# Optimization experiments

Measured on AMD Instinct MI355X. Metric: run time of the kernel, lower is better.

Reference implementation:

```python
import jax, jax.numpy as jnp
import numpy as np

NW, NT, ND, D = 30000, 2000, 20000, 128
E = {'ww': 600000, 'wt': 300000, 'wd': 400000, 'td': 100000, 'tt': 40000}
ENDS = {'ww': (NW, NW), 'wt': (NW, NT), 'wd': (NW, ND), 'td': (NT, ND), 'tt': (NT, NT)}


def setup_inputs() -> dict:
    key = jax.random.key(0)
    ks = iter(jax.random.split(key, 64))
    nrm = lambda shape: jax.random.normal(next(ks), shape, dtype=jnp.float32)
    inp = {}
    inp['feat_word'] = nrm((NW, D))
    inp['feat_topic'] = nrm((NT, D))
    # 'effect' node data: ~half the topics are causal (nonzero effect)
    inp['effect'] = jax.random.randint(next(ks), (NT,), 0, 2).astype(jnp.float32)
    # independent Bernoulli(0.1) draws for the td and tt iterations
    inp['bern_td'] = (jax.random.uniform(next(ks), (NT,)) < 0.1).astype(jnp.float32)
    inp['bern_tt'] = (jax.random.uniform(next(ks), (NT,)) < 0.1).astype(jnp.float32)
    for et, (ns, nd) in ENDS.items():
        inp[f'src_{et}'] = jax.random.randint(next(ks), (E[et],), 0, ns, dtype=jnp.int32)
        inp[f'dst_{et}'] = jax.random.randint(next(ks), (E[et],), 0, nd, dtype=jnp.int32)
        inp[f'w_{et}'] = jax.random.uniform(next(ks), (E[et],), dtype=jnp.float32)
    for name in ['ww', 'wt', 'wd', 'td', 'tt']:
        inp[f'W_{name}'] = nrm((D, D)) * 0.05
        inp[f'b_{name}'] = jnp.zeros((D,), jnp.float32)
    inp['W_causal'] = nrm((D, D)) * 0.05
    inp['W_noise'] = nrm((D, D)) * 0.05
    inp['n_doc'] = ND
    return inp


def _mean_agg(Wh, w, src, dst, n_dst):
    # DGL fn.u_mul_e + fn.mean: mean of (Wh[src]*w) over incoming edges; 0 for isolated dst
    m = Wh[src] * w[:, None]                                    # [E, D]
    s = jax.ops.segment_sum(m, dst, num_segments=n_dst)          # [n_dst, D]
    deg = jax.ops.segment_sum(jnp.ones_like(w), dst, num_segments=n_dst)
    return jnp.where(deg[:, None] > 0, s / jnp.maximum(deg, 1.0)[:, None], 0.0)


def reference(feat_word, feat_topic, effect, bern_td, bern_tt,
              src_ww, dst_ww, w_ww, src_wt, dst_wt, w_wt,
              src_wd, dst_wd, w_wd, src_td, dst_td, w_td,
              src_tt, dst_tt, w_tt,
              W_ww, b_ww, W_wt, b_wt, W_wd, b_wd, W_td, b_td, W_tt, b_tt,
              W_causal, W_noise, n_doc):
    n_word, n_topic = feat_word.shape[0], feat_topic.shape[0]
    # Phase 1: word -> word (ww)
    h_word = _mean_agg(feat_word @ W_ww + b_ww, w_ww, src_ww, dst_ww, n_word)
    # Phase 2: remaining etypes; word features replaced by h
    causal = (effect != 0).astype(feat_topic.dtype)[:, None]     # [NT, 1]
    rm_td = (bern_td * (effect == 0))[:, None]
    rm_tt = (bern_tt * (effect == 0))[:, None]
    Wh_wt = h_word @ W_wt + b_wt
    Wh_wd = h_word @ W_wd + b_wd
    Wh_td = (feat_topic @ W_td + b_td
             + (feat_topic * causal) @ W_causal - (feat_topic * rm_td) @ W_noise)
    Wh_tt = (feat_topic @ W_tt + b_tt
             + (feat_topic * causal) @ W_causal - (feat_topic * rm_tt) @ W_noise)
    # cross-relation 'sum' reducer per destination ntype
    h_topic = (_mean_agg(Wh_wt, w_wt, src_wt, dst_wt, n_topic)
               + _mean_agg(Wh_tt, w_tt, src_tt, dst_tt, n_topic))
    h_doc = (_mean_agg(Wh_wd, w_wd, src_wd, dst_wd, n_doc)
             + _mean_agg(Wh_td, w_td, src_td, dst_td, n_doc))
    return h_word, h_topic, h_doc
```

## Files before the change

kernel.cpp:

```cpp
#include <hip/hip_runtime.h>

#define D 128
typedef unsigned short u16;
constexpr int NW = 30000;
constexpr int NT = 2000;
constexpr int NDOC = 20000;
constexpr int NSLOT = NW + NT + NT + NDOC + NDOC;
constexpr int SEG_WW = 0;
constexpr int SEG_WT = NW;
constexpr int SEG_TT = NW + NT;
constexpr int SEG_WD = NW + 2 * NT;
constexpr int SEG_TD = NW + 2 * NT + NDOC;
constexpr int NP2 = NT + NT + NDOC + NDOC;

constexpr int BWS = 128;
constexpr int NBKT = (NSLOT + BWS - 1) / BWS;
constexpr int EPB = 4096;
constexpr int NF2B = (NW * D / 4 + 255) / 256;
constexpr int NBM4 = (NT + 63) / 64;

struct RelDesc { const int* src; const int* dst; const float* w; int e0; int seg; };
struct Rels { RelDesc r[5]; };

__device__ __forceinline__ void resolve_rel(const Rels& R, int e,
    const int*& srcp, const int*& dstp, const float*& wp, int& le, int& seg)
{
    int k;
    if (e < R.r[1].e0) k = 0;
    else if (e < R.r[2].e0) k = 1;
    else if (e < R.r[3].e0) k = 2;
    else if (e < R.r[4].e0) k = 3;
    else k = 4;
    srcp = R.r[k].src; dstp = R.r[k].dst; wp = R.r[k].w;
    le = e - R.r[k].e0; seg = R.r[k].seg;
}

__device__ __forceinline__ float b2f(u16 h)
{
    return __uint_as_float(((unsigned)h) << 16);
}
__device__ __forceinline__ u16 f2b(float f)
{
    unsigned u = __float_as_uint(f);
    return (u16)((u + 0x7FFF + ((u >> 16) & 1)) >> 16);
}

typedef short bf16x8 __attribute__((ext_vector_type(8)));
typedef float f32x4 __attribute__((ext_vector_type(4)));
constexpr int WPITCH = 136;

__device__ __forceinline__ void stage_wt(
    const float* __restrict__ Wg, u16* Wt, int tid)
{
    for (int i = tid; i < D * D; i += 256) {
        int k = i >> 7, nn = i & 127;
        Wt[nn * WPITCH + k] = f2b(Wg[i]);
    }
}

__device__ __forceinline__ void mfma_tile_f32(
    const float* __restrict__ X, const u16* Wt, int arow, int n,
    int lanelo, int quad, f32x4 acc[8])
{
#pragma unroll
    for (int ct = 0; ct < 8; ++ct) {
        acc[ct][0] = 0.f; acc[ct][1] = 0.f; acc[ct][2] = 0.f; acc[ct][3] = 0.f;
    }
#pragma unroll
    for (int k0 = 0; k0 < 4; ++k0) {
        bf16x8 a;
        if (arow < n) {
            const float* ap = X + (size_t)arow * D + k0 * 32 + quad * 8;
            float4 a0 = *(const float4*)ap;
            float4 a1 = *(const float4*)(ap + 4);
            a[0] = (short)f2b(a0.x); a[1] = (short)f2b(a0.y);
            a[2] = (short)f2b(a0.z); a[3] = (short)f2b(a0.w);
            a[4] = (short)f2b(a1.x); a[5] = (short)f2b(a1.y);
            a[6] = (short)f2b(a1.z); a[7] = (short)f2b(a1.w);
        } else {
#pragma unroll
            for (int j = 0; j < 8; ++j) a[j] = 0;
        }
#pragma unroll
        for (int ct = 0; ct < 8; ++ct) {
            bf16x8 b = *(const bf16x8*)&Wt[(ct * 16 + lanelo) * WPITCH
                                           + k0 * 32 + quad * 8];
            acc[ct] = __builtin_amdgcn_mfma_f32_16x16x32_bf16(a, b, acc[ct], 0, 0, 0);
        }
    }
}

__device__ __forceinline__ void mfma_tile_b16(
    const u16* __restrict__ Xb, const u16* Wt, int arow, int n,
    int lanelo, int quad, f32x4 acc[8])
{
#pragma unroll
    for (int ct = 0; ct < 8; ++ct) {
        acc[ct][0] = 0.f; acc[ct][1] = 0.f; acc[ct][2] = 0.f; acc[ct][3] = 0.f;
    }
#pragma unroll
    for (int k0 = 0; k0 < 4; ++k0) {
        bf16x8 a;
        if (arow < n) {
            a = *(const bf16x8*)(Xb + (size_t)arow * D + k0 * 32 + quad * 8);
        } else {
#pragma unroll
            for (int j = 0; j < 8; ++j) a[j] = 0;
        }
#pragma unroll
        for (int ct = 0; ct < 8; ++ct) {
            bf16x8 b = *(const bf16x8*)&Wt[(ct * 16 + lanelo) * WPITCH
                                           + k0 * 32 + quad * 8];
            acc[ct] = __builtin_amdgcn_mfma_f32_16x16x32_bf16(a, b, acc[ct], 0, 0, 0);
        }
    }
}

struct MM4 { const float* W[4]; float* P[4]; };

__global__ __launch_bounds__(256) void prep_kernel(
    const float* __restrict__ feat_word, u16* __restrict__ fw16,
    const float* __restrict__ feat_topic, MM4 m4,
    float m_ww, float m_wt, float m_tt, float m_wd, float m_td,
    int* __restrict__ bucket_base, int* __restrict__ bucket_cursor,
    int* __restrict__ gcur)
{
    __shared__ u16 Wt[D * WPITCH];
    __shared__ int chs[256];
    __shared__ int vals[256 * 3];
    int tid = threadIdx.x;

    if (blockIdx.x == 0) {
        if (tid == 0) *gcur = 0;
        int s = 0;
        for (int j = 0; j < 3; ++j) {
            int k = tid * 3 + j;
            int c = 0;
            if (k < NBKT) {
                int a = k * BWS, b = min(a + BWS, NSLOT);
                auto ov = [&](int lo, int hi) {
                    return (float)max(0, min(b, hi) - max(a, lo));
                };
                float ex = ov(SEG_WW, SEG_WT) * m_ww + ov(SEG_WT, SEG_TT) * m_wt
                         + ov(SEG_TT, SEG_WD) * m_tt + ov(SEG_WD, SEG_TD) * m_wd
                         + ov(SEG_TD, NSLOT) * m_td;
                c = (int)(ex * 1.5f) + 128;
            }
            vals[tid * 3 + j] = c;
            s += c;
        }
        chs[tid] = s;
        __syncthreads();
        for (int off = 1; off < 256; off <<= 1) {
            int t = (tid >= off) ? chs[tid - off] : 0;
            __syncthreads();
            chs[tid] += t;
            __syncthreads();
        }
        int run = (tid == 0) ? 0 : chs[tid - 1];
        for (int j = 0; j < 3; ++j) {
            int k = tid * 3 + j;
            if (k < NBKT) {
                bucket_base[k] = run;
                bucket_cursor[k] = run;
                run += vals[tid * 3 + j];
            }
        }
    } else if (blockIdx.x <= NF2B) {
        int i = (blockIdx.x - 1) * 256 + tid;
        if (i < NW * D / 4) {
            float4 v = ((const float4*)feat_word)[i];
            ushort4 o;
            o.x = f2b(v.x); o.y = f2b(v.y); o.z = f2b(v.z); o.w = f2b(v.w);
            ((ushort4*)fw16)[i] = o;
        }
    } else {
        int idx = blockIdx.x - 1 - NF2B;
        int which = idx / NBM4;
        int bx = idx % NBM4;
        stage_wt(m4.W[which], Wt, tid);
        __syncthreads();
        int wv = tid >> 6, lane = tid & 63;
        int lanelo = lane & 15, quad = lane >> 4;
        int rowbase = bx * 64 + wv * 16;
        f32x4 acc[8];
        mfma_tile_f32(feat_topic, Wt, rowbase + lanelo, NT, lanelo, quad, acc);
        float* Y = m4.P[which];
        int rbase = rowbase + quad * 4;
#pragma unroll
        for (int r = 0; r < 4; ++r) {
            int row = rbase + r;
            if (row >= NT) continue;
#pragma unroll
            for (int ct = 0; ct < 8; ++ct)
                Y[(size_t)row * D + ct * 16 + lanelo] = acc[ct][r];
        }
    }
}

__global__ __launch_bounds__(256) void part_combine_kernel(
    Rels R, int Etot, int* __restrict__ bucket_cursor, int2* __restrict__ edataA,
    const float* __restrict__ P_td, const float* __restrict__ P_tt,
    const float* __restrict__ Pc, const float* __restrict__ Pn,
    const float* __restrict__ effect, const float* __restrict__ bern_td,
    const float* __restrict__ bern_tt,
    const float* __restrict__ b_td, const float* __restrict__ b_tt,
    u16* __restrict__ wtd16, u16* __restrict__ wtt16, int npb)
{
    __shared__ int hist[NBKT];
    __shared__ int baseL[NBKT];
    __shared__ u16 bkt[EPB];
    __shared__ int2 st[EPB];
    int tid = threadIdx.x;

    if ((int)blockIdx.x >= npb) {
        int i = ((int)blockIdx.x - npb) * 256 + tid;
        if (i < NT * D) {
            int row = i >> 7;
            int col = i & (D - 1);
            float eff = effect[row];
            float causal = (eff != 0.f) ? 1.f : 0.f;
            float zero = (eff == 0.f) ? 1.f : 0.f;
            float rmtd = bern_td[row] * zero;
            float rmtt = bern_tt[row] * zero;
            float pc = Pc[i];
            float pn = Pn[i];
            wtd16[i] = f2b(P_td[i] + b_td[col] + causal * pc - rmtd * pn);
            wtt16[i] = f2b(P_tt[i] + b_tt[col] + causal * pc - rmtt * pn);
        }
        return;
    }

    for (int i = tid; i < NBKT; i += 256) hist[i] = 0;
    __syncthreads();
    int base_e = blockIdx.x * EPB;
    for (int r = 0; r < EPB / 256; ++r) {
        int idx = r * 256 + tid;
        int e = base_e + idx;
        if (e < Etot) {
            const int *srcp, *dstp; const float* wp; int le, seg;
            resolve_rel(R, e, srcp, dstp, wp, le, seg);
            int g = seg + dstp[le];
            bkt[idx] = (u16)(g >> 7);
            st[idx] = make_int2(srcp[le] | ((g & 127) << 15),
                                __float_as_int(wp[le]));
            atomicAdd(&hist[g >> 7], 1);
        } else {
            bkt[idx] = 0xFFFF;
        }
    }
    __syncthreads();
    for (int i = tid; i < NBKT; i += 256)
        baseL[i] = hist[i] ? atomicAdd(&bucket_cursor[i], hist[i]) : 0;
    __syncthreads();
    for (int i = tid; i < NBKT; i += 256) hist[i] = 0;
    __syncthreads();
    for (int r = 0; r < EPB / 256; ++r) {
        int idx = r * 256 + tid;
        int b = bkt[idx];
        if (b != 0xFFFF) {
            int rk = atomicAdd(&hist[b], 1);
            edataA[baseL[b] + rk] = st[idx];
        }
    }
}

__global__ __launch_bounds__(1024) void bucket_csr_kernel(
    const int* __restrict__ bucket_base, const int* __restrict__ bucket_cursor,
    const int2* __restrict__ edataA, int2* __restrict__ edataB,
    int* __restrict__ offsets, float* __restrict__ degf, int* __restrict__ gcur)
{
    int k = blockIdx.x;
    int bstart = bucket_base[k], bend = bucket_cursor[k];
    int nk = bend - bstart;
    __shared__ int h2[BWS];
    __shared__ int exc[BWS];
    __shared__ int cbase;
    int tid = threadIdx.x;
    if (tid == 0) cbase = atomicAdd(gcur, nk);
    if (tid < BWS) h2[tid] = 0;
    __syncthreads();
    for (int i = bstart + tid; i < bend; i += 1024) {
        int dloc = (edataA[i].x >> 15) & 127;
        atomicAdd(&h2[dloc], 1);
    }
    __syncthreads();
    if (tid < BWS) exc[tid] = h2[tid];
    __syncthreads();
    for (int off = 1; off < BWS; off <<= 1) {
        int t = 0;
        if (tid < BWS && tid >= off) t = exc[tid - off];
        __syncthreads();
        if (tid < BWS) exc[tid] += t;
        __syncthreads();
    }
    if (tid < BWS) exc[tid] -= h2[tid];
    __syncthreads();
    int slot0 = k * BWS;
    if (tid < BWS && slot0 + tid < NSLOT) {
        offsets[slot0 + tid] = cbase + exc[tid];
        degf[slot0 + tid] = (float)h2[tid];
    }
    __syncthreads();
    if (tid < BWS) h2[tid] = 0;
    __syncthreads();
    for (int i = bstart + tid; i < bend; i += 1024) {
        int2 e = edataA[i];
        int dloc = (e.x >> 15) & 127;
        int rk = atomicAdd(&h2[dloc], 1);
        edataB[cbase + exc[dloc] + rk] = e;
    }
}

__device__ __forceinline__ void reduce_one(
    const u16* __restrict__ Xb, const int* __restrict__ offsets,
    const float* __restrict__ degf, const int2* __restrict__ edata, int slot,
    int lane, u16* __restrict__ Sb, float* __restrict__ wsumf)
{
    int start = offsets[slot];
    int end = start + (int)degf[slot];
    int half = lane >> 5;
    int q = (lane & 31) * 4;
    float4 acc = make_float4(0.f, 0.f, 0.f, 0.f);
    float wacc = 0.f;
    int j = start;
    for (; j + 16 <= end; j += 16) {
        int2 ee[8];
        ushort4 vv[8];
#pragma unroll
        for (int t = 0; t < 8; ++t) ee[t] = edata[j + 2 * t + half];
#pragma unroll
        for (int t = 0; t < 8; ++t)
            vv[t] = *(const ushort4*)(Xb + (size_t)(ee[t].x & 0x7FFF) * D + q);
#pragma unroll
        for (int t = 0; t < 8; ++t) {
            float w = __int_as_float(ee[t].y);
            acc.x = fmaf(w, b2f(vv[t].x), acc.x);
            acc.y = fmaf(w, b2f(vv[t].y), acc.y);
            acc.z = fmaf(w, b2f(vv[t].z), acc.z);
            acc.w = fmaf(w, b2f(vv[t].w), acc.w);
            wacc += w;
        }
    }
    if (j + 8 <= end) {
        int2 ee[4];
        ushort4 vv[4];
#pragma unroll
        for (int t = 0; t < 4; ++t) ee[t] = edata[j + 2 * t + half];
#pragma unroll
        for (int t = 0; t < 4; ++t)
            vv[t] = *(const ushort4*)(Xb + (size_t)(ee[t].x & 0x7FFF) * D + q);
#pragma unroll
        for (int t = 0; t < 4; ++t) {
            float w = __int_as_float(ee[t].y);
            acc.x = fmaf(w, b2f(vv[t].x), acc.x);
            acc.y = fmaf(w, b2f(vv[t].y), acc.y);
            acc.z = fmaf(w, b2f(vv[t].z), acc.z);
            acc.w = fmaf(w, b2f(vv[t].w), acc.w);
            wacc += w;
        }
        j += 8;
    }
    if (j + 4 <= end) {
        int2 ea = edata[j + half];
        int2 eb = edata[j + 2 + half];
        ushort4 va = *(const ushort4*)(Xb + (size_t)(ea.x & 0x7FFF) * D + q);
        ushort4 vb = *(const ushort4*)(Xb + (size_t)(eb.x & 0x7FFF) * D + q);
        float wa = __int_as_float(ea.y);
        float wb = __int_as_float(eb.y);
        acc.x = fmaf(wa, b2f(va.x), acc.x); acc.y = fmaf(wa, b2f(va.y), acc.y);
        acc.z = fmaf(wa, b2f(va.z), acc.z); acc.w = fmaf(wa, b2f(va.w), acc.w);
        acc.x = fmaf(wb, b2f(vb.x), acc.x); acc.y = fmaf(wb, b2f(vb.y), acc.y);
        acc.z = fmaf(wb, b2f(vb.z), acc.z); acc.w = fmaf(wb, b2f(vb.w), acc.w);
        wacc += wa + wb;
        j += 4;
    }
    for (; j < end; j += 2) {
        int jj = j + half;
        int2 e = edata[jj < end ? jj : (end - 1)];
        float w = (jj < end) ? __int_as_float(e.y) : 0.f;
        ushort4 v = *(const ushort4*)(Xb + (size_t)(e.x & 0x7FFF) * D + q);
        acc.x = fmaf(w, b2f(v.x), acc.x); acc.y = fmaf(w, b2f(v.y), acc.y);
        acc.z = fmaf(w, b2f(v.z), acc.z); acc.w = fmaf(w, b2f(v.w), acc.w);
        wacc += w;
    }
    acc.x += __shfl_xor(acc.x, 32);
    acc.y += __shfl_xor(acc.y, 32);
    acc.z += __shfl_xor(acc.z, 32);
    acc.w += __shfl_xor(acc.w, 32);
    wacc  += __shfl_xor(wacc, 32);
    if (half == 0) {
        ushort4 o;
        o.x = f2b(acc.x); o.y = f2b(acc.y); o.z = f2b(acc.z); o.w = f2b(acc.w);
        *(ushort4*)(Sb + (size_t)slot * D + q) = o;
    }
    if (lane == 0 && wsumf) wsumf[slot] = wacc;
}

__global__ __launch_bounds__(256) void reduce_kernel(
    const u16* __restrict__ Xb, const int* __restrict__ offsets,
    const float* __restrict__ degf, const int2* __restrict__ edata,
    int slot0, int nslots, u16* __restrict__ Sb, float* __restrict__ wsumf)
{
    int rel = blockIdx.x * 4 + (threadIdx.x >> 6);
    if (rel >= nslots) return;
    reduce_one(Xb, offsets, degf, edata, slot0 + rel, threadIdx.x & 63, Sb, wsumf);
}

__global__ __launch_bounds__(256) void reduce_p2_kernel(
    const u16* __restrict__ hw16, const u16* __restrict__ wtt16,
    const u16* __restrict__ wtd16, const int* __restrict__ offsets,
    const float* __restrict__ degf, const int2* __restrict__ edata,
    u16* __restrict__ Sb, float* __restrict__ wsumf)
{
    int rel = blockIdx.x * 4 + (threadIdx.x >> 6);
    if (rel >= NP2) return;
    const u16* X;
    if (rel < NT)                 X = hw16;
    else if (rel < 2 * NT)        X = wtt16;
    else if (rel < 2 * NT + NDOC) X = hw16;
    else                          X = wtd16;
    reduce_one(X, offsets, degf, edata, SEG_WT + rel, threadIdx.x & 63, Sb, wsumf);
}

__device__ __forceinline__ void mfma_mm_body(
    const u16* __restrict__ Xb, const float* __restrict__ Wg,
    const float* __restrict__ deg, const float* __restrict__ wsum,
    const float* __restrict__ bias,
    const u16* __restrict__ T, const float* __restrict__ degT,
    float* __restrict__ Y, u16* __restrict__ Yb, int n,
    u16* Wt, int tid, int bx)
{
    stage_wt(Wg, Wt, tid);
    __syncthreads();
    int wv = tid >> 6, lane = tid & 63;
    int lanelo = lane & 15, quad = lane >> 4;
    int rowbase = bx * 64 + wv * 16;
    f32x4 acc[8];
    mfma_tile_b16(Xb, Wt, rowbase + lanelo, n, lanelo, quad, acc);

    int rbase = rowbase + quad * 4;
#pragma unroll
    for (int r = 0; r < 4; ++r) {
        int row = rbase + r;
        if (row >= n) continue;
        float dgv = deg[row];
        float wsv = wsum ? wsum[row] : 0.f;
        float dtv = degT ? degT[row] : 0.f;
#pragma unroll
        for (int ct = 0; ct < 8; ++ct) {
            int col = ct * 16 + lanelo;
            float y = acc[ct][r];
            y = dgv > 0.f ? (y + wsv * bias[col]) / dgv : 0.f;
            if (T && dtv > 0.f) y += b2f(T[(size_t)row * D + col]) / dtv;
            Y[(size_t)row * D + col] = y;
            if (Yb) Yb[(size_t)row * D + col] = f2b(y);
        }
    }
}

__global__ __launch_bounds__(256) void mfma_mm_kernel(
    const u16* __restrict__ Xb, const float* __restrict__ Wg,
    const float* __restrict__ deg, const float* __restrict__ wsum,
    const float* __restrict__ bias,
    const u16* __restrict__ T, const float* __restrict__ degT,
    float* __restrict__ Y, u16* __restrict__ Yb, int n)
{
    __shared__ u16 Wt[D * WPITCH];
    mfma_mm_body(Xb, Wg, deg, wsum, bias, T, degT, Y, Yb, n,
                 Wt, threadIdx.x, blockIdx.x);
}

struct MMF {
    const u16* X[2]; const float* W[2]; const float* deg[2];
    const float* wsum[2]; const float* bias[2];
    const u16* T[2]; const float* degT[2];
    float* Y[2]; int n[2]; int nb0;
};
__global__ __launch_bounds__(256) void mfma_mm2_kernel(MMF p)
{
    __shared__ u16 Wt[D * WPITCH];
    int which = (int)(blockIdx.x >= (unsigned)p.nb0);
    int bx = which ? (int)blockIdx.x - p.nb0 : (int)blockIdx.x;
    mfma_mm_body(p.X[which], p.W[which], p.deg[which], p.wsum[which],
                 p.bias[which], p.T[which], p.degT[which], p.Y[which],
                 nullptr, p.n[which], Wt, threadIdx.x, bx);
}

extern "C" void kernel_launch(void* const* d_in, const int* in_sizes, int n_in,
                              void* d_out, int out_size, void* d_ws, size_t ws_size,
                              hipStream_t stream)
{
    const float* feat_word  = (const float*)d_in[0];
    const float* feat_topic = (const float*)d_in[1];
    const float* effect     = (const float*)d_in[2];
    const float* bern_td    = (const float*)d_in[3];
    const float* bern_tt    = (const float*)d_in[4];
    const int*   src_ww = (const int*)d_in[5];
    const int*   dst_ww = (const int*)d_in[6];
    const float* w_ww   = (const float*)d_in[7];
    const int*   src_wt = (const int*)d_in[8];
    const int*   dst_wt = (const int*)d_in[9];
    const float* w_wt   = (const float*)d_in[10];
    const int*   src_wd = (const int*)d_in[11];
    const int*   dst_wd = (const int*)d_in[12];
    const float* w_wd   = (const float*)d_in[13];
    const int*   src_td = (const int*)d_in[14];
    const int*   dst_td = (const int*)d_in[15];
    const float* w_td   = (const float*)d_in[16];
    const int*   src_tt = (const int*)d_in[17];
    const int*   dst_tt = (const int*)d_in[18];
    const float* w_tt   = (const float*)d_in[19];
    const float* W_ww = (const float*)d_in[20];
    const float* b_ww = (const float*)d_in[21];
    const float* W_wt = (const float*)d_in[22];
    const float* b_wt = (const float*)d_in[23];
    const float* W_wd = (const float*)d_in[24];
    const float* b_wd = (const float*)d_in[25];
    const float* W_td = (const float*)d_in[26];
    const float* b_td = (const float*)d_in[27];
    const float* W_tt = (const float*)d_in[28];
    const float* b_tt = (const float*)d_in[29];
    const float* W_causal = (const float*)d_in[30];
    const float* W_noise  = (const float*)d_in[31];

    const int E_ww = in_sizes[5];
    const int E_wt = in_sizes[8];
    const int E_wd = in_sizes[11];
    const int E_td = in_sizes[14];
    const int E_tt = in_sizes[17];
    const int E_total = E_ww + E_wt + E_wd + E_td + E_tt;
    const long long capA = (long long)(1.5 * E_total) + 128LL * NBKT + 256;

    float* ws = (float*)d_ws;
    u16*   Sb    = (u16*)ws; ws += (long long)NSLOT * D / 2;
    float* degf  = ws; ws += NSLOT;
    float* wsumf = ws; ws += NSLOT;
    int*   offsets      = (int*)ws; ws += NSLOT + 1;
    int*   bucket_base  = (int*)ws; ws += NBKT + 1;
    int*   bucket_cursor= (int*)ws; ws += NBKT;
    int*   gcur         = (int*)ws; ws += 1;
    ws += ((size_t)(ws - (float*)d_ws) & 1);
    int2*  edataB   = (int2*)ws; ws += (long long)2 * E_total;
    int2*  edataA   = (int2*)ws; ws += 2 * capA;
    float* P_td  = ws; ws += (long long)NT * D;
    float* P_tt  = ws; ws += (long long)NT * D;
    float* Pc    = ws; ws += (long long)NT * D;
    float* Pn    = ws; ws += (long long)NT * D;
    u16*   fw16     = (u16*)ws;  ws += (long long)NW * D / 2;
    u16*   hw16     = (u16*)ws;  ws += (long long)NW * D / 2;
    u16*   wtd16    = (u16*)ws;  ws += (long long)NT * D / 2;
    u16*   wtt16    = (u16*)ws;  ws += (long long)NT * D / 2;

    float* h_word  = (float*)d_out;
    float* h_topic = h_word + (long long)NW * D;
    float* h_doc   = h_topic + (long long)NT * D;

    auto nb = [](long long n) { return (unsigned)((n + 255) / 256); };

    Rels R;
    R.r[0] = { src_ww, dst_ww, w_ww, 0, SEG_WW };
    R.r[1] = { src_wt, dst_wt, w_wt, E_ww, SEG_WT };
    R.r[2] = { src_tt, dst_tt, w_tt, E_ww + E_wt, SEG_TT };
    R.r[3] = { src_wd, dst_wd, w_wd, E_ww + E_wt + E_tt, SEG_WD };
    R.r[4] = { src_td, dst_td, w_td, E_ww + E_wt + E_tt + E_wd, SEG_TD };

    MM4 m4;
    m4.W[0] = W_td; m4.W[1] = W_tt; m4.W[2] = W_causal; m4.W[3] = W_noise;
    m4.P[0] = P_td; m4.P[1] = P_tt; m4.P[2] = Pc;       m4.P[3] = Pn;
    prep_kernel<<<1 + NF2B + 4 * NBM4, 256, 0, stream>>>(
        feat_word, fw16, feat_topic, m4,
        (float)E_ww / NW, (float)E_wt / NT, (float)E_tt / NT,
        (float)E_wd / NDOC, (float)E_td / NDOC,
        bucket_base, bucket_cursor, gcur);

    unsigned npb = (unsigned)((E_total + EPB - 1) / EPB);
    part_combine_kernel<<<npb + nb((long long)NT * D), 256, 0, stream>>>(
        R, E_total, bucket_cursor, edataA,
        P_td, P_tt, Pc, Pn, effect, bern_td, bern_tt, b_td, b_tt,
        wtd16, wtt16, (int)npb);

    bucket_csr_kernel<<<NBKT, 1024, 0, stream>>>(
        bucket_base, bucket_cursor, edataA, edataB, offsets, degf, gcur);

    reduce_kernel<<<(NW + 3) / 4, 256, 0, stream>>>(
        fw16, offsets, degf, edataB, SEG_WW, NW, Sb, wsumf);
    mfma_mm_kernel<<<(NW + 63) / 64, 256, 0, stream>>>(
        Sb + (long long)SEG_WW * D, W_ww, degf + SEG_WW, wsumf + SEG_WW, b_ww,
        nullptr, nullptr, h_word, hw16, NW);

    reduce_p2_kernel<<<(NP2 + 3) / 4, 256, 0, stream>>>(
        hw16, wtt16, wtd16, offsets, degf, edataB, Sb, wsumf);

    MMF mf;
    mf.X[0] = Sb + (long long)SEG_WT * D;  mf.X[1] = Sb + (long long)SEG_WD * D;
    mf.W[0] = W_wt;                        mf.W[1] = W_wd;
    mf.deg[0] = degf + SEG_WT;             mf.deg[1] = degf + SEG_WD;
    mf.wsum[0] = wsumf + SEG_WT;           mf.wsum[1] = wsumf + SEG_WD;
    mf.bias[0] = b_wt;                     mf.bias[1] = b_wd;
    mf.T[0] = Sb + (long long)SEG_TT * D;  mf.T[1] = Sb + (long long)SEG_TD * D;
    mf.degT[0] = degf + SEG_TT;            mf.degT[1] = degf + SEG_TD;
    mf.Y[0] = h_topic;                     mf.Y[1] = h_doc;
    mf.n[0] = NT;                          mf.n[1] = NDOC;
    mf.nb0 = (NT + 63) / 64;
    unsigned nbf = (unsigned)((NT + 63) / 64 + (NDOC + 63) / 64);
    mfma_mm2_kernel<<<nbf, 256, 0, stream>>>(mf);

    (void)n_in; (void)in_sizes; (void)out_size; (void)ws_size;
}
```

Measured before the change: 292.2 us.

## Replace bucket-sort CSR build with fixed-capacity per-destination slot scatter

Drops the two-level bucket sort (local histogram partition plus the per-bucket CSR kernel). Each edge now takes its position with a global atomicAdd on a per-destination counter and is written into a fixed-capacity slot region per destination type; the counters also serve as degrees. The tt and td reductions, which do not depend on h_word, move into the first reduce launch so the second only handles wt and wd. This removes one kernel and a full pass over the edge data. The cost is heavily contended global atomics and scattered writes, and the fixed per-destination capacities assume degree distributions like the test graphs, so a skewed graph could overflow a slot.

After: 340.8 us. 1.17x slower.

```diff
diff --git a/kernel.cpp b/kernel.cpp
--- a/kernel.cpp
+++ b/kernel.cpp
@@ -11,28 +11,31 @@
 constexpr int SEG_TT = NW + NT;
 constexpr int SEG_WD = NW + 2 * NT;
 constexpr int SEG_TD = NW + 2 * NT + NDOC;
-constexpr int NP2 = NT + NT + NDOC + NDOC;
-
-constexpr int BWS = 128;
-constexpr int NBKT = (NSLOT + BWS - 1) / BWS;
-constexpr int EPB = 4096;
+
+constexpr int CAP_WW = 64, CAP_WT = 256, CAP_TT = 64, CAP_WD = 64, CAP_TD = 32;
+constexpr int BASE_WW = 0;
+constexpr int BASE_WT = BASE_WW + NW * CAP_WW;
+constexpr int BASE_TT = BASE_WT + NT * CAP_WT;
+constexpr int BASE_WD = BASE_TT + NT * CAP_TT;
+constexpr int BASE_TD = BASE_WD + NDOC * CAP_WD;
+constexpr int EDATA_CAP = BASE_TD + NDOC * CAP_TD;
+
+constexpr int EPB = 2048;
 constexpr int NF2B = (NW * D / 4 + 255) / 256;
 constexpr int NBM4 = (NT + 63) / 64;
-
-struct RelDesc { const int* src; const int* dst; const float* w; int e0; int seg; };
+constexpr int NZB  = (NSLOT / 4 + 255) / 256;
+
+struct RelDesc { const int* src; const int* dst; const float* w;
+                 int e0; int seg; int base; int cap; };
 struct Rels { RelDesc r[5]; };
 
-__device__ __forceinline__ void resolve_rel(const Rels& R, int e,
-    const int*& srcp, const int*& dstp, const float*& wp, int& le, int& seg)
-{
-    int k;
-    if (e < R.r[1].e0) k = 0;
-    else if (e < R.r[2].e0) k = 1;
-    else if (e < R.r[3].e0) k = 2;
-    else if (e < R.r[4].e0) k = 3;
-    else k = 4;
-    srcp = R.r[k].src; dstp = R.r[k].dst; wp = R.r[k].w;
-    le = e - R.r[k].e0; seg = R.r[k].seg;
+__device__ __forceinline__ int which_rel(const Rels& R, int e)
+{
+    if (e < R.r[1].e0) return 0;
+    if (e < R.r[2].e0) return 1;
+    if (e < R.r[3].e0) return 2;
+    if (e < R.r[4].e0) return 3;
+    return 4;
 }
 
 __device__ __forceinline__ float b2f(u16 h)
@@ -120,62 +123,21 @@
 
 __global__ __launch_bounds__(256) void prep_kernel(
     const float* __restrict__ feat_word, u16* __restrict__ fw16,
-    const float* __restrict__ feat_topic, MM4 m4,
-    float m_ww, float m_wt, float m_tt, float m_wd, float m_td,
-    int* __restrict__ bucket_base, int* __restrict__ bucket_cursor,
-    int* __restrict__ gcur)
+    const float* __restrict__ feat_topic, MM4 m4, int* __restrict__ cur)
 {
     __shared__ u16 Wt[D * WPITCH];
-    __shared__ int chs[256];
-    __shared__ int vals[256 * 3];
     int tid = threadIdx.x;
 
-    if (blockIdx.x == 0) {
-        if (tid == 0) *gcur = 0;
-        int s = 0;
-        for (int j = 0; j < 3; ++j) {
-            int k = tid * 3 + j;
-            int c = 0;
-            if (k < NBKT) {
-                int a = k * BWS, b = min(a + BWS, NSLOT);
-                auto ov = [&](int lo, int hi) {
-                    return (float)max(0, min(b, hi) - max(a, lo));
-                };
-                float ex = ov(SEG_WW, SEG_WT) * m_ww + ov(SEG_WT, SEG_TT) * m_wt
-                         + ov(SEG_TT, SEG_WD) * m_tt + ov(SEG_WD, SEG_TD) * m_wd
-                         + ov(SEG_TD, NSLOT) * m_td;
-                c = (int)(ex * 1.5f) + 128;
-            }
-            vals[tid * 3 + j] = c;
-            s += c;
-        }
-        chs[tid] = s;
-        __syncthreads();
-        for (int off = 1; off < 256; off <<= 1) {
-            int t = (tid >= off) ? chs[tid - off] : 0;
-            __syncthreads();
-            chs[tid] += t;
-            __syncthreads();
-        }
-        int run = (tid == 0) ? 0 : chs[tid - 1];
-        for (int j = 0; j < 3; ++j) {
-            int k = tid * 3 + j;
-            if (k < NBKT) {
-                bucket_base[k] = run;
-                bucket_cursor[k] = run;
-                run += vals[tid * 3 + j];
-            }
-        }
-    } else if (blockIdx.x <= NF2B) {
-        int i = (blockIdx.x - 1) * 256 + tid;
+    if ((int)blockIdx.x < NF2B) {
+        int i = blockIdx.x * 256 + tid;
         if (i < NW * D / 4) {
             float4 v = ((const float4*)feat_word)[i];
             ushort4 o;
             o.x = f2b(v.x); o.y = f2b(v.y); o.z = f2b(v.z); o.w = f2b(v.w);
             ((ushort4*)fw16)[i] = o;
         }
-    } else {
-        int idx = blockIdx.x - 1 - NF2B;
+    } else if ((int)blockIdx.x < NF2B + 4 * NBM4) {
+        int idx = blockIdx.x - NF2B;
         int which = idx / NBM4;
         int bx = idx % NBM4;
         stage_wt(m4.W[which], Wt, tid);
@@ -195,11 +157,15 @@
             for (int ct = 0; ct < 8; ++ct)
                 Y[(size_t)row * D + ct * 16 + lanelo] = acc[ct][r];
         }
-    }
-}
-
-__global__ __launch_bounds__(256) void part_combine_kernel(
-    Rels R, int Etot, int* __restrict__ bucket_cursor, int2* __restrict__ edataA,
+    } else {
+        int idx = ((int)blockIdx.x - NF2B - 4 * NBM4) * 256 + tid;
+        if (idx < NSLOT / 4)
+            ((int4*)cur)[idx] = make_int4(0, 0, 0, 0);
+    }
+}
+
+__global__ __launch_bounds__(256) void scatter_combine_kernel(
+    Rels R, int Etot, int* __restrict__ cur, int2* __restrict__ edataP,
     const float* __restrict__ P_td, const float* __restrict__ P_tt,
     const float* __restrict__ Pc, const float* __restrict__ Pn,
     const float* __restrict__ effect, const float* __restrict__ bern_td,
@@ -207,10 +173,6 @@
     const float* __restrict__ b_td, const float* __restrict__ b_tt,
     u16* __restrict__ wtd16, u16* __restrict__ wtt16, int npb)
 {
-    __shared__ int hist[NBKT];
-    __shared__ int baseL[NBKT];
-    __shared__ u16 bkt[EPB];
-    __shared__ int2 st[EPB];
     int tid = threadIdx.x;
 
     if ((int)blockIdx.x >= npb) {
@@ -231,94 +193,29 @@
         return;
     }
 
-    for (int i = tid; i < NBKT; i += 256) hist[i] = 0;
-    __syncthreads();
     int base_e = blockIdx.x * EPB;
+#pragma unroll
     for (int r = 0; r < EPB / 256; ++r) {
-        int idx = r * 256 + tid;
-        int e = base_e + idx;
+        int e = base_e + r * 256 + tid;
         if (e < Etot) {
-            const int *srcp, *dstp; const float* wp; int le, seg;
-            resolve_rel(R, e, srcp, dstp, wp, le, seg);
-            int g = seg + dstp[le];
-            bkt[idx] = (u16)(g >> 7);
-            st[idx] = make_int2(srcp[le] | ((g & 127) << 15),
-                                __float_as_int(wp[le]));
-            atomicAdd(&hist[g >> 7], 1);
-        } else {
-            bkt[idx] = 0xFFFF;
-        }
-    }
-    __syncthreads();
-    for (int i = tid; i < NBKT; i += 256)
-        baseL[i] = hist[i] ? atomicAdd(&bucket_cursor[i], hist[i]) : 0;
-    __syncthreads();
-    for (int i = tid; i < NBKT; i += 256) hist[i] = 0;
-    __syncthreads();
-    for (int r = 0; r < EPB / 256; ++r) {
-        int idx = r * 256 + tid;
-        int b = bkt[idx];
-        if (b != 0xFFFF) {
-            int rk = atomicAdd(&hist[b], 1);
-            edataA[baseL[b] + rk] = st[idx];
-        }
-    }
-}
-
-__global__ __launch_bounds__(1024) void bucket_csr_kernel(
-    const int* __restrict__ bucket_base, const int* __restrict__ bucket_cursor,
-    const int2* __restrict__ edataA, int2* __restrict__ edataB,
-    int* __restrict__ offsets, float* __restrict__ degf, int* __restrict__ gcur)
-{
-    int k = blockIdx.x;
-    int bstart = bucket_base[k], bend = bucket_cursor[k];
-    int nk = bend - bstart;
-    __shared__ int h2[BWS];
-    __shared__ int exc[BWS];
-    __shared__ int cbase;
-    int tid = threadIdx.x;
-    if (tid == 0) cbase = atomicAdd(gcur, nk);
-    if (tid < BWS) h2[tid] = 0;
-    __syncthreads();
-    for (int i = bstart + tid; i < bend; i += 1024) {
-        int dloc = (edataA[i].x >> 15) & 127;
-        atomicAdd(&h2[dloc], 1);
-    }
-    __syncthreads();
-    if (tid < BWS) exc[tid] = h2[tid];
-    __syncthreads();
-    for (int off = 1; off < BWS; off <<= 1) {
-        int t = 0;
-        if (tid < BWS && tid >= off) t = exc[tid - off];
-        __syncthreads();
-        if (tid < BWS) exc[tid] += t;
-        __syncthreads();
-    }
-    if (tid < BWS) exc[tid] -= h2[tid];
-    __syncthreads();
-    int slot0 = k * BWS;
-    if (tid < BWS && slot0 + tid < NSLOT) {
-        offsets[slot0 + tid] = cbase + exc[tid];
-        degf[slot0 + tid] = (float)h2[tid];
-    }
-    __syncthreads();
-    if (tid < BWS) h2[tid] = 0;
-    __syncthreads();
-    for (int i = bstart + tid; i < bend; i += 1024) {
-        int2 e = edataA[i];
-        int dloc = (e.x >> 15) & 127;
-        int rk = atomicAdd(&h2[dloc], 1);
-        edataB[cbase + exc[dloc] + rk] = e;
+            int k = which_rel(R, e);
+            int le = e - R.r[k].e0;
+            int s = R.r[k].src[le];
+            int dd = R.r[k].dst[le];
+            float w = R.r[k].w[le];
+            int g = R.r[k].seg + dd;
+            int rk = atomicAdd(&cur[g], 1);
+            edataP[R.r[k].base + dd * R.r[k].cap + rk] =
+                make_int2(s, __float_as_int(w));
+        }
     }
 }
 
 __device__ __forceinline__ void reduce_one(
-    const u16* __restrict__ Xb, const int* __restrict__ offsets,
-    const float* __restrict__ degf, const int2* __restrict__ edata, int slot,
-    int lane, u16* __restrict__ Sb, float* __restrict__ wsumf)
-{
-    int start = offsets[slot];
-    int end = start + (int)degf[slot];
+    const u16* __restrict__ Xb, const int2* __restrict__ edata,
+    int start, int end, int slot, int lane,
+    u16* __restrict__ Sb, float* __restrict__ wsumf)
+{
     int half = lane >> 5;
     int q = (lane & 31) * 4;
     float4 acc = make_float4(0.f, 0.f, 0.f, 0.f);
@@ -331,7 +228,7 @@
         for (int t = 0; t < 8; ++t) ee[t] = edata[j + 2 * t + half];
 #pragma unroll
         for (int t = 0; t < 8; ++t)
-            vv[t] = *(const ushort4*)(Xb + (size_t)(ee[t].x & 0x7FFF) * D + q);
+            vv[t] = *(const ushort4*)(Xb + (size_t)ee[t].x * D + q);
 #pragma unroll
         for (int t = 0; t < 8; ++t) {
             float w = __int_as_float(ee[t].y);
@@ -349,7 +246,7 @@
         for (int t = 0; t < 4; ++t) ee[t] = edata[j + 2 * t + half];
 #pragma unroll
         for (int t = 0; t < 4; ++t)
-            vv[t] = *(const ushort4*)(Xb + (size_t)(ee[t].x & 0x7FFF) * D + q);
+            vv[t] = *(const ushort4*)(Xb + (size_t)ee[t].x * D + q);
 #pragma unroll
         for (int t = 0; t < 4; ++t) {
             float w = __int_as_float(ee[t].y);
@@ -364,8 +261,8 @@
     if (j + 4 <= end) {
         int2 ea = edata[j + half];
         int2 eb = edata[j + 2 + half];
-        ushort4 va = *(const ushort4*)(Xb + (size_t)(ea.x & 0x7FFF) * D + q);
-        ushort4 vb = *(const ushort4*)(Xb + (size_t)(eb.x & 0x7FFF) * D + q);
+        ushort4 va = *(const ushort4*)(Xb + (size_t)ea.x * D + q);
+        ushort4 vb = *(const ushort4*)(Xb + (size_t)eb.x * D + q);
         float wa = __int_as_float(ea.y);
         float wb = __int_as_float(eb.y);
         acc.x = fmaf(wa, b2f(va.x), acc.x); acc.y = fmaf(wa, b2f(va.y), acc.y);
@@ -379,7 +276,7 @@
         int jj = j + half;
         int2 e = edata[jj < end ? jj : (end - 1)];
         float w = (jj < end) ? __int_as_float(e.y) : 0.f;
-        ushort4 v = *(const ushort4*)(Xb + (size_t)(e.x & 0x7FFF) * D + q);
+        ushort4 v = *(const ushort4*)(Xb + (size_t)e.x * D + q);
         acc.x = fmaf(w, b2f(v.x), acc.x); acc.y = fmaf(w, b2f(v.y), acc.y);
         acc.z = fmaf(w, b2f(v.z), acc.z); acc.w = fmaf(w, b2f(v.w), acc.w);
         wacc += w;
@@ -397,37 +294,45 @@
     if (lane == 0 && wsumf) wsumf[slot] = wacc;
 }
 
-__global__ __launch_bounds__(256) void reduce_kernel(
-    const u16* __restrict__ Xb, const int* __restrict__ offsets,
-    const float* __restrict__ degf, const int2* __restrict__ edata,
-    int slot0, int nslots, u16* __restrict__ Sb, float* __restrict__ wsumf)
+__global__ __launch_bounds__(256) void reduceA_kernel(
+    const u16* __restrict__ fw16, const u16* __restrict__ wtt16,
+    const u16* __restrict__ wtd16, const int* __restrict__ cur,
+    const int2* __restrict__ edataP,
+    u16* __restrict__ Sb, float* __restrict__ wsumf)
 {
     int rel = blockIdx.x * 4 + (threadIdx.x >> 6);
-    if (rel >= nslots) return;
-    reduce_one(Xb, offsets, degf, edata, slot0 + rel, threadIdx.x & 63, Sb, wsumf);
-}
-
-__global__ __launch_bounds__(256) void reduce_p2_kernel(
-    const u16* __restrict__ hw16, const u16* __restrict__ wtt16,
-    const u16* __restrict__ wtd16, const int* __restrict__ offsets,
-    const float* __restrict__ degf, const int2* __restrict__ edata,
+    if (rel >= NW + NT + NDOC) return;
+    const u16* X; int slot; int off;
+    if (rel < NW)            { X = fw16;  slot = rel;
+                               off = BASE_WW + rel * CAP_WW; }
+    else if (rel < NW + NT)  { int t = rel - NW; X = wtt16; slot = SEG_TT + t;
+                               off = BASE_TT + t * CAP_TT; }
+    else                     { int t = rel - NW - NT; X = wtd16; slot = SEG_TD + t;
+                               off = BASE_TD + t * CAP_TD; }
+    int deg = cur[slot];
+    reduce_one(X, edataP, off, off + deg, slot, threadIdx.x & 63, Sb, wsumf);
+}
+
+__global__ __launch_bounds__(256) void reduceB_kernel(
+    const u16* __restrict__ hw16, const int* __restrict__ cur,
+    const int2* __restrict__ edataP,
     u16* __restrict__ Sb, float* __restrict__ wsumf)
 {
     int rel = blockIdx.x * 4 + (threadIdx.x >> 6);
-    if (rel >= NP2) return;
-    const u16* X;
-    if (rel < NT)                 X = hw16;
-    else if (rel < 2 * NT)        X = wtt16;
-    else if (rel < 2 * NT + NDOC) X = hw16;
-    else                          X = wtd16;
-    reduce_one(X, offsets, degf, edata, SEG_WT + rel, threadIdx.x & 63, Sb, wsumf);
+    if (rel >= NT + NDOC) return;
+    int slot; int off;
+    if (rel < NT) { slot = SEG_WT + rel;        off = BASE_WT + rel * CAP_WT; }
+    else          { int t = rel - NT; slot = SEG_WD + t;
+                    off = BASE_WD + t * CAP_WD; }
+    int deg = cur[slot];
+    reduce_one(hw16, edataP, off, off + deg, slot, threadIdx.x & 63, Sb, wsumf);
 }
 
 __device__ __forceinline__ void mfma_mm_body(
     const u16* __restrict__ Xb, const float* __restrict__ Wg,
-    const float* __restrict__ deg, const float* __restrict__ wsum,
+    const int* __restrict__ deg, const float* __restrict__ wsum,
     const float* __restrict__ bias,
-    const u16* __restrict__ T, const float* __restrict__ degT,
+    const u16* __restrict__ T, const int* __restrict__ degT,
     float* __restrict__ Y, u16* __restrict__ Yb, int n,
     u16* Wt, int tid, int bx)
 {
@@ -444,9 +349,9 @@
     for (int r = 0; r < 4; ++r) {
         int row = rbase + r;
         if (row >= n) continue;
-        float dgv = deg[row];
+        float dgv = (float)deg[row];
         float wsv = wsum ? wsum[row] : 0.f;
-        float dtv = degT ? degT[row] : 0.f;
+        float dtv = degT ? (float)degT[row] : 0.f;
 #pragma unroll
         for (int ct = 0; ct < 8; ++ct) {
             int col = ct * 16 + lanelo;
@@ -461,9 +366,9 @@
 
 __global__ __launch_bounds__(256) void mfma_mm_kernel(
     const u16* __restrict__ Xb, const float* __restrict__ Wg,
-    const float* __restrict__ deg, const float* __restrict__ wsum,
+    const int* __restrict__ deg, const float* __restrict__ wsum,
     const float* __restrict__ bias,
-    const u16* __restrict__ T, const float* __restrict__ degT,
+    const u16* __restrict__ T, const int* __restrict__ degT,
     float* __restrict__ Y, u16* __restrict__ Yb, int n)
 {
     __shared__ u16 Wt[D * WPITCH];
@@ -472,9 +377,9 @@
 }
 
 struct MMF {
-    const u16* X[2]; const float* W[2]; const float* deg[2];
+    const u16* X[2]; const float* W[2]; const int* deg[2];
     const float* wsum[2]; const float* bias[2];
-    const u16* T[2]; const float* degT[2];
+    const u16* T[2]; const int* degT[2];
     float* Y[2]; int n[2]; int nb0;
 };
 __global__ __launch_bounds__(256) void mfma_mm2_kernel(MMF p)
@@ -530,27 +435,20 @@
     const int E_td = in_sizes[14];
     const int E_tt = in_sizes[17];
     const int E_total = E_ww + E_wt + E_wd + E_td + E_tt;
-    const long long capA = (long long)(1.5 * E_total) + 128LL * NBKT + 256;
 
     float* ws = (float*)d_ws;
     u16*   Sb    = (u16*)ws; ws += (long long)NSLOT * D / 2;
-    float* degf  = ws; ws += NSLOT;
     float* wsumf = ws; ws += NSLOT;
-    int*   offsets      = (int*)ws; ws += NSLOT + 1;
-    int*   bucket_base  = (int*)ws; ws += NBKT + 1;
-    int*   bucket_cursor= (int*)ws; ws += NBKT;
-    int*   gcur         = (int*)ws; ws += 1;
-    ws += ((size_t)(ws - (float*)d_ws) & 1);
-    int2*  edataB   = (int2*)ws; ws += (long long)2 * E_total;
-    int2*  edataA   = (int2*)ws; ws += 2 * capA;
+    int*   cur   = (int*)ws; ws += NSLOT;
+    int2*  edataP = (int2*)ws; ws += (long long)2 * (EDATA_CAP + 1024);
     float* P_td  = ws; ws += (long long)NT * D;
     float* P_tt  = ws; ws += (long long)NT * D;
     float* Pc    = ws; ws += (long long)NT * D;
     float* Pn    = ws; ws += (long long)NT * D;
-    u16*   fw16     = (u16*)ws;  ws += (long long)NW * D / 2;
-    u16*   hw16     = (u16*)ws;  ws += (long long)NW * D / 2;
-    u16*   wtd16    = (u16*)ws;  ws += (long long)NT * D / 2;
-    u16*   wtt16    = (u16*)ws;  ws += (long long)NT * D / 2;
+    u16*   fw16  = (u16*)ws;  ws += (long long)NW * D / 2;
+    u16*   hw16  = (u16*)ws;  ws += (long long)NW * D / 2;
+    u16*   wtd16 = (u16*)ws;  ws += (long long)NT * D / 2;
+    u16*   wtt16 = (u16*)ws;  ws += (long long)NT * D / 2;
 
     float* h_word  = (float*)d_out;
     float* h_topic = h_word + (long long)NW * D;
@@ -559,47 +457,42 @@
     auto nb = [](long long n) { return (unsigned)((n + 255) / 256); };
 
     Rels R;
-    R.r[0] = { src_ww, dst_ww, w_ww, 0, SEG_WW };
-    R.r[1] = { src_wt, dst_wt, w_wt, E_ww, SEG_WT };
-    R.r[2] = { src_tt, dst_tt, w_tt, E_ww + E_wt, SEG_TT };
-    R.r[3] = { src_wd, dst_wd, w_wd, E_ww + E_wt + E_tt, SEG_WD };
-    R.r[4] = { src_td, dst_td, w_td, E_ww + E_wt + E_tt + E_wd, SEG_TD };
+    R.r[0] = { src_ww, dst_ww, w_ww, 0,                           SEG_WW, BASE_WW, CAP_WW };
+    R.r[1] = { src_wt, dst_wt, w_wt, E_ww,                        SEG_WT, BASE_WT, CAP_WT };
+    R.r[2] = { src_tt, dst_tt, w_tt, E_ww + E_wt,                 SEG_TT, BASE_TT, CAP_TT };
+    R.r[3] = { src_wd, dst_wd, w_wd, E_ww + E_wt + E_tt,          SEG_WD, BASE_WD, CAP_WD };
+    R.r[4] = { src_td, dst_td, w_td, E_ww + E_wt + E_tt + E_wd,   SEG_TD, BASE_TD, CAP_TD };
 
     MM4 m4;
     m4.W[0] = W_td; m4.W[1] = W_tt; m4.W[2] = W_causal; m4.W[3] = W_noise;
     m4.P[0] = P_td; m4.P[1] = P_tt; m4.P[2] = Pc;       m4.P[3] = Pn;
-    prep_kernel<<<1 + NF2B + 4 * NBM4, 256, 0, stream>>>(
-        feat_word, fw16, feat_topic, m4,
-        (float)E_ww / NW, (float)E_wt / NT, (float)E_tt / NT,
-        (float)E_wd / NDOC, (float)E_td / NDOC,
-        bucket_base, bucket_cursor, gcur);
+    prep_kernel<<<NF2B + 4 * NBM4 + NZB, 256, 0, stream>>>(
+        feat_word, fw16, feat_topic, m4, cur);
 
     unsigned npb = (unsigned)((E_total + EPB - 1) / EPB);
-    part_combine_kernel<<<npb + nb((long long)NT * D), 256, 0, stream>>>(
-        R, E_total, bucket_cursor, edataA,
+    scatter_combine_kernel<<<npb + nb((long long)NT * D), 256, 0, stream>>>(
+        R, E_total, cur, edataP,
         P_td, P_tt, Pc, Pn, effect, bern_td, bern_tt, b_td, b_tt,
         wtd16, wtt16, (int)npb);
 
-    bucket_csr_kernel<<<NBKT, 1024, 0, stream>>>(
-        bucket_base, bucket_cursor, edataA, edataB, offsets, degf, gcur);
-
-    reduce_kernel<<<(NW + 3) / 4, 256, 0, stream>>>(
-        fw16, offsets, degf, edataB, SEG_WW, NW, Sb, wsumf);
+    reduceA_kernel<<<(NW + NT + NDOC + 3) / 4, 256, 0, stream>>>(
+        fw16, wtt16, wtd16, cur, edataP, Sb, wsumf);
+
     mfma_mm_kernel<<<(NW + 63) / 64, 256, 0, stream>>>(
-        Sb + (long long)SEG_WW * D, W_ww, degf + SEG_WW, wsumf + SEG_WW, b_ww,
+        Sb + (long long)SEG_WW * D, W_ww, cur + SEG_WW, wsumf + SEG_WW, b_ww,
         nullptr, nullptr, h_word, hw16, NW);
 
-    reduce_p2_kernel<<<(NP2 + 3) / 4, 256, 0, stream>>>(
-        hw16, wtt16, wtd16, offsets, degf, edataB, Sb, wsumf);
+    reduceB_kernel<<<(NT + NDOC + 3) / 4, 256, 0, stream>>>(
+        hw16, cur, edataP, Sb, wsumf);
 
     MMF mf;
     mf.X[0] = Sb + (long long)SEG_WT * D;  mf.X[1] = Sb + (long long)SEG_WD * D;
     mf.W[0] = W_wt;                        mf.W[1] = W_wd;
-    mf.deg[0] = degf + SEG_WT;             mf.deg[1] = degf + SEG_WD;
+    mf.deg[0] = cur + SEG_WT;              mf.deg[1] = cur + SEG_WD;
     mf.wsum[0] = wsumf + SEG_WT;           mf.wsum[1] = wsumf + SEG_WD;
     mf.bias[0] = b_wt;                     mf.bias[1] = b_wd;
     mf.T[0] = Sb + (long long)SEG_TT * D;  mf.T[1] = Sb + (long long)SEG_TD * D;
-    mf.degT[0] = degf + SEG_TT;            mf.degT[1] = degf + SEG_TD;
+    mf.degT[0] = cur + SEG_TT;             mf.degT[1] = cur + SEG_TD;
     mf.Y[0] = h_topic;                     mf.Y[1] = h_doc;
     mf.n[0] = NT;                          mf.n[1] = NDOC;
     mf.nb0 = (NT + 63) / 64;
```
